# Optimization experiments

Hardware: AMD Instinct MI355X
Metric: run time of the kernel (lower is better)

The kernel has to match this reference:

```python
import jax, jax.numpy as jnp
import numpy as np

E = 100_000      # number of edges
KMAX = 16        # neighbors (quadruplet basis edges) per edge, exact in this setup
E_NB = E * KMAX  # total neighbor entries
D_EDGE, D_SBF, D_QUAD = 128, 32, 32
INV_SQRT_2 = 0.7071067811865475


def setup_inputs() -> dict:
    key = jax.random.key(0)
    ks = jax.random.split(key, 8)
    m_st = jax.random.normal(ks[0], (E, D_EDGE), dtype=jnp.float32)
    sbf = jax.random.normal(ks[1], (E_NB, D_SBF), dtype=jnp.float32)
    # consistent ragged structure: each edge has exactly KMAX neighbor entries
    edge_nb_idx = jnp.repeat(jnp.arange(E, dtype=jnp.int64), KMAX)
    edge_nb_ragged_idx = jnp.tile(jnp.arange(KMAX, dtype=jnp.int64), E)
    idx_swap = jax.random.permutation(ks[2], E).astype(jnp.int64)
    # parameters (Dense layers are bias-free per the module)
    W_down = jax.random.normal(ks[3], (D_EDGE, D_QUAD), dtype=jnp.float32) / np.sqrt(D_EDGE)
    W_bil = jax.random.normal(ks[4], (D_QUAD, D_SBF, D_QUAD), dtype=jnp.float32) / np.sqrt(D_QUAD * D_SBF)
    W_up_st = jax.random.normal(ks[5], (D_QUAD, D_EDGE), dtype=jnp.float32) / np.sqrt(D_QUAD)
    W_up_ts = jax.random.normal(ks[6], (D_QUAD, D_EDGE), dtype=jnp.float32) / np.sqrt(D_QUAD)
    scale_sbf = jnp.ones((1,), dtype=jnp.float32)  # ScaleFactor (fitted scalar, 1.0 at init)
    return {
        "m_st": m_st, "sbf": sbf, "idx_swap": idx_swap,
        "edge_nb_idx": edge_nb_idx, "edge_nb_ragged_idx": edge_nb_ragged_idx,
        "W_down": W_down, "W_bil": W_bil, "W_up_st": W_up_st,
        "W_up_ts": W_up_ts, "scale_sbf": scale_sbf,
    }


def reference(m_st, sbf, idx_swap, edge_nb_idx, edge_nb_ragged_idx,
              W_down, W_bil, W_up_st, W_up_ts, scale_sbf):
    # mlp_down: Dense(no bias) + SiLU  -> (E, Q)
    m = jax.nn.silu(m_st @ W_down)
    # gather edge embeddings to neighbor entries -> (E_NB, Q)
    m_nb = m[edge_nb_idx]
    # EfficientInteractionBilinear: scatter ragged entries into dense
    # (E, Kmax, *) buffers, then bilinear contraction over neighbors.
    m2 = jnp.zeros((E, KMAX, D_QUAD), m.dtype).at[edge_nb_idx, edge_nb_ragged_idx].set(m_nb)
    s2 = jnp.zeros((E, KMAX, D_SBF), sbf.dtype).at[edge_nb_idx, edge_nb_ragged_idx].set(sbf)
    sum_k = jnp.einsum("eks,ekq->esq", s2, m2)           # (E, S, Q)
    x = jnp.einsum("esq,qso->eo", sum_k, W_bil)          # (E, Q)
    # ScaleFactor: multiply by fitted scalar
    x = x * scale_sbf[0]
    # up-projections + SiLU, swap-add, normalize
    x_st = jax.nn.silu(x @ W_up_st)
    x_ts = jax.nn.silu(x @ W_up_ts)[idx_swap]
    return (x_st + x_ts) * INV_SQRT_2
```

## Files before the change

### kernel.cpp

```cpp
#include <hip/hip_runtime.h>
#include <hip/hip_bf16.h>

#define E_EDGES 100000
#define KMAXN   16
#define D_EDGE  128
#define D_SBF   32
#define D_QUAD  32
#define NTILES  6250
#define SP      36

typedef __bf16 bf16x8 __attribute__((ext_vector_type(8)));
typedef float  f32x4  __attribute__((ext_vector_type(4)));

__device__ __forceinline__ float silu_f(float x) {
    return x / (1.0f + __expf(-x));
}

__global__ __launch_bounds__(256) void kprep(
        const float* __restrict__ W_down,
        const float* __restrict__ W_bil,
        __bf16* __restrict__ Wd16,
        __bf16* __restrict__ Wb16)
{
    const int t = blockIdx.x * 256 + threadIdx.x;
    if (t < 4096) {
        const int o   = t & 31;
        const int tmp = t >> 5;
        const int qh  = tmp & 3;
        const int s   = tmp >> 2;
        bf16x8 u;
        #pragma unroll
        for (int ql = 0; ql < 8; ql++)
            u[ql] = (__bf16)W_bil[(qh*8 + ql)*1024 + s*32 + o];
        *(bf16x8*)(Wb16 + (size_t)t * 8) = u;
    } else if (t < 4096 + 512) {
        const int t2   = t - 4096;
        const int n15  = t2 & 15;
        const int quad = (t2 >> 4) & 3;
        const int nt   = (t2 >> 6) & 1;
        const int kk   = t2 >> 7;
        bf16x8 u;
        #pragma unroll
        for (int j = 0; j < 8; j++)
            u[j] = (__bf16)W_down[(kk*32 + quad*8 + j)*32 + nt*16 + n15];
        *(bf16x8*)(Wd16 + (size_t)t2 * 8) = u;
    }
}

__global__ __launch_bounds__(256, 4) void k012_fused(
        const float* __restrict__ sbf,
        const float* __restrict__ m_st,
        const __bf16* __restrict__ Wd16,
        const __bf16* __restrict__ Wb16,
        const float* __restrict__ scale_sbf,
        float* __restrict__ ws_x)
{
    __shared__ __align__(16) float Slds[4][16 * SP];
    __shared__ __align__(16) float Mlds[4][16 * SP];

    const int lane = threadIdx.x & 63;
    const int n15  = lane & 15;
    const int quad = lane >> 4;
    const int wid  = threadIdx.x >> 6;
    const int tile = blockIdx.x * 4 + wid;
    if (tile >= NTILES) return;
    const int eb = tile * 16;
    const int e8 = lane >> 3;
    const int c  = lane & 7;

    float* Sw = Slds[wid];
    float* Mw = Mlds[wid];

    #pragma unroll
    for (int eh = 0; eh < 2; eh++) {
        const float* p = sbf + (size_t)(eb + eh*8 + e8) * (KMAXN * D_SBF) + c * 4;
        float ax = 0.f, ay = 0.f, az = 0.f, aw = 0.f;
        #pragma unroll
        for (int k = 0; k < KMAXN; k++) {
            float4 v = *(const float4*)(p + k * D_SBF);
            ax += v.x; ay += v.y; az += v.z; aw += v.w;
        }
        float4 r = {ax, ay, az, aw};
        *(float4*)(Sw + (eh*8 + e8) * SP + c * 4) = r;
    }

    const bf16x8* Wdq = (const bf16x8*)Wd16;
    const float* arow = m_st + (size_t)(eb + n15) * 128 + quad * 8;
    f32x4 acc0 = {0.f, 0.f, 0.f, 0.f};
    f32x4 acc1 = {0.f, 0.f, 0.f, 0.f};
    #pragma unroll
    for (int kk = 0; kk < 4; kk++) {
        float4 p0 = *(const float4*)(arow + kk*32);
        float4 p1 = *(const float4*)(arow + kk*32 + 4);
        bf16x8 a;
        a[0]=(__bf16)p0.x; a[1]=(__bf16)p0.y; a[2]=(__bf16)p0.z; a[3]=(__bf16)p0.w;
        a[4]=(__bf16)p1.x; a[5]=(__bf16)p1.y; a[6]=(__bf16)p1.z; a[7]=(__bf16)p1.w;
        bf16x8 b0 = Wdq[(kk*2 + 0)*64 + quad*16 + n15];
        bf16x8 b1 = Wdq[(kk*2 + 1)*64 + quad*16 + n15];
        acc0 = __builtin_amdgcn_mfma_f32_16x16x32_bf16(a, b0, acc0, 0, 0, 0);
        acc1 = __builtin_amdgcn_mfma_f32_16x16x32_bf16(a, b1, acc1, 0, 0, 0);
    }
    #pragma unroll
    for (int reg = 0; reg < 4; reg++) {
        Mw[(quad*4 + reg)*SP +      n15] = silu_f(acc0[reg]);
        Mw[(quad*4 + reg)*SP + 16 + n15] = silu_f(acc1[reg]);
    }

    asm volatile("s_waitcnt lgkmcnt(0)" ::: "memory");

    const float* mrow = Mw + n15*SP + quad*8;
    float4 m0 = *(const float4*)mrow;
    float4 m1 = *(const float4*)(mrow + 4);
    float mj[8] = {m0.x, m0.y, m0.z, m0.w, m1.x, m1.y, m1.z, m1.w};
    const float* srow = Sw + n15*SP;
    const bf16x8* Bq = (const bf16x8*)Wb16;

    f32x4 xc0 = {0.f, 0.f, 0.f, 0.f};
    f32x4 xc1 = {0.f, 0.f, 0.f, 0.f};
    #pragma unroll
    for (int kk = 0; kk < 32; kk++) {
        const float sv = srow[kk];
        bf16x8 a;
        #pragma unroll
        for (int j = 0; j < 8; j++) a[j] = (__bf16)(sv * mj[j]);
        bf16x8 b0 = Bq[(kk*4 + quad)*32 +      n15];
        bf16x8 b1 = Bq[(kk*4 + quad)*32 + 16 + n15];
        xc0 = __builtin_amdgcn_mfma_f32_16x16x32_bf16(a, b0, xc0, 0, 0, 0);
        xc1 = __builtin_amdgcn_mfma_f32_16x16x32_bf16(a, b1, xc1, 0, 0, 0);
    }

    const float scale = scale_sbf[0];
    #pragma unroll
    for (int reg = 0; reg < 4; reg++) {
        const int eo = eb + quad*4 + reg;
        ws_x[(size_t)eo*32 +      n15] = xc0[reg] * scale;
        ws_x[(size_t)eo*32 + 16 + n15] = xc1[reg] * scale;
    }
}

__global__ __launch_bounds__(256) void k3_up(
        const float* __restrict__ ws_x,
        const int*   __restrict__ idx_swap,
        const float* __restrict__ W_up_st,
        const float* __restrict__ W_up_ts,
        float* __restrict__ out)
{
    const int lane = threadIdx.x & 63;
    const int n15  = lane & 15;
    const int quad = lane >> 4;
    const int wave = blockIdx.x * 4 + (threadIdx.x >> 6);
    const int nwav = gridDim.x * 4;

    bf16x8 bst[8], bts[8];
    #pragma unroll
    for (int nt = 0; nt < 8; nt++) {
        bf16x8 a, b;
        #pragma unroll
        for (int j = 0; j < 8; j++) {
            a[j] = (__bf16)W_up_st[(quad*8 + j) * 128 + nt*16 + n15];
            b[j] = (__bf16)W_up_ts[(quad*8 + j) * 128 + nt*16 + n15];
        }
        bst[nt] = a; bts[nt] = b;
    }

    const float cinv = 0.70710678118654752440f;

    for (int tile = wave; tile < NTILES; tile += nwav) {
        const int eb = tile * 16;
        const int e  = eb + n15;
        const int esw = idx_swap[e];

        const float* xr = ws_x + (size_t)e   * 32 + quad * 8;
        const float* xs = ws_x + (size_t)esw * 32 + quad * 8;
        float4 r0 = *(const float4*)xr, r1 = *(const float4*)(xr + 4);
        float4 s0 = *(const float4*)xs, s1 = *(const float4*)(xs + 4);

        bf16x8 ast, ats;
        ast[0]=(__bf16)r0.x; ast[1]=(__bf16)r0.y; ast[2]=(__bf16)r0.z; ast[3]=(__bf16)r0.w;
        ast[4]=(__bf16)r1.x; ast[5]=(__bf16)r1.y; ast[6]=(__bf16)r1.z; ast[7]=(__bf16)r1.w;
        ats[0]=(__bf16)s0.x; ats[1]=(__bf16)s0.y; ats[2]=(__bf16)s0.z; ats[3]=(__bf16)s0.w;
        ats[4]=(__bf16)s1.x; ats[5]=(__bf16)s1.y; ats[6]=(__bf16)s1.z; ats[7]=(__bf16)s1.w;

        f32x4 accst[8], accts[8];
        #pragma unroll
        for (int nt = 0; nt < 8; nt++) {
            f32x4 z = {0.f, 0.f, 0.f, 0.f};
            accst[nt] = __builtin_amdgcn_mfma_f32_16x16x32_bf16(ast, bst[nt], z, 0, 0, 0);
            accts[nt] = __builtin_amdgcn_mfma_f32_16x16x32_bf16(ats, bts[nt], z, 0, 0, 0);
        }

        #pragma unroll
        for (int nt = 0; nt < 8; nt++) {
            #pragma unroll
            for (int reg = 0; reg < 4; reg++) {
                const int eo = eb + quad*4 + reg;
                out[(size_t)eo * 128 + nt*16 + n15] =
                    (silu_f(accst[nt][reg]) + silu_f(accts[nt][reg])) * cinv;
            }
        }
    }
}

extern "C" void kernel_launch(void* const* d_in, const int* in_sizes, int n_in,
                              void* d_out, int out_size, void* d_ws, size_t ws_size,
                              hipStream_t stream)
{
    const float* m_st      = (const float*)d_in[0];
    const float* sbf       = (const float*)d_in[1];
    const int*   idx_swap  = (const int*)  d_in[2];
    const float* W_down    = (const float*)d_in[5];
    const float* W_bil     = (const float*)d_in[6];
    const float* W_up_st   = (const float*)d_in[7];
    const float* W_up_ts   = (const float*)d_in[8];
    const float* scale_sbf = (const float*)d_in[9];
    float* out = (float*)d_out;

    const size_t nEQ = (size_t)E_EDGES * D_QUAD;
    float*  ws_x = (float*)d_ws;
    __bf16* Wd16 = (__bf16*)(ws_x + nEQ);
    __bf16* Wb16 = Wd16 + 512 * 8;

    hipLaunchKernelGGL(kprep,      dim3(18),   dim3(256), 0, stream,
                       W_down, W_bil, Wd16, Wb16);
    hipLaunchKernelGGL(k012_fused, dim3(1563), dim3(256), 0, stream,
                       sbf, m_st, Wd16, Wb16, scale_sbf, ws_x);
    hipLaunchKernelGGL(k3_up,      dim3(1024), dim3(256), 0, stream,
                       ws_x, idx_swap, W_up_st, W_up_ts, out);
}
```

Before: 383.5 us.

## Split sbf neighbor-sum into separate streaming kernel before fused bilinear

Moves the reduction of sbf over the 16 neighbors out of the fused MFMA kernel into a standalone, fully parallel kernel that writes per-edge sums to workspace. The fused kernel then loads the 32 summed values per edge straight into registers instead of staging them through LDS. The aim is to let the dominant 205MB sbf stream run at full occupancy, separate from the MFMA kernel's limited occupancy. The cost is an extra launch and an additional round trip of the summed buffer through global memory.

```diff
diff --git a/kernel.cpp b/kernel.cpp
--- a/kernel.cpp
+++ b/kernel.cpp
@@ -14,6 +14,25 @@
 
 __device__ __forceinline__ float silu_f(float x) {
     return x / (1.0f + __expf(-x));
+}
+
+__global__ __launch_bounds__(256) void k0_ssum(
+        const float* __restrict__ sbf,
+        float* __restrict__ ssum)
+{
+    const int tid = blockIdx.x * 256 + threadIdx.x;
+    if (tid >= E_EDGES * 8) return;
+    const int e = tid >> 3;
+    const int c = tid & 7;
+    const float* p = sbf + (size_t)e * (KMAXN * D_SBF) + c * 4;
+    float ax = 0.f, ay = 0.f, az = 0.f, aw = 0.f;
+    #pragma unroll
+    for (int k = 0; k < KMAXN; k++) {
+        float4 v = *(const float4*)(p + k * D_SBF);
+        ax += v.x; ay += v.y; az += v.z; aw += v.w;
+    }
+    float4 r = {ax, ay, az, aw};
+    *(float4*)(ssum + (size_t)e * D_SBF + c * 4) = r;
 }
 
 __global__ __launch_bounds__(256) void kprep(
@@ -47,15 +66,14 @@
     }
 }
 
-__global__ __launch_bounds__(256, 4) void k012_fused(
-        const float* __restrict__ sbf,
+__global__ __launch_bounds__(256, 4) void k12_fused(
+        const float* __restrict__ ssum,
         const float* __restrict__ m_st,
         const __bf16* __restrict__ Wd16,
         const __bf16* __restrict__ Wb16,
         const float* __restrict__ scale_sbf,
         float* __restrict__ ws_x)
 {
-    __shared__ __align__(16) float Slds[4][16 * SP];
     __shared__ __align__(16) float Mlds[4][16 * SP];
 
     const int lane = threadIdx.x & 63;
@@ -65,24 +83,8 @@
     const int tile = blockIdx.x * 4 + wid;
     if (tile >= NTILES) return;
     const int eb = tile * 16;
-    const int e8 = lane >> 3;
-    const int c  = lane & 7;
-
-    float* Sw = Slds[wid];
+
     float* Mw = Mlds[wid];
-
-    #pragma unroll
-    for (int eh = 0; eh < 2; eh++) {
-        const float* p = sbf + (size_t)(eb + eh*8 + e8) * (KMAXN * D_SBF) + c * 4;
-        float ax = 0.f, ay = 0.f, az = 0.f, aw = 0.f;
-        #pragma unroll
-        for (int k = 0; k < KMAXN; k++) {
-            float4 v = *(const float4*)(p + k * D_SBF);
-            ax += v.x; ay += v.y; az += v.z; aw += v.w;
-        }
-        float4 r = {ax, ay, az, aw};
-        *(float4*)(Sw + (eh*8 + e8) * SP + c * 4) = r;
-    }
 
     const bf16x8* Wdq = (const bf16x8*)Wd16;
     const float* arow = m_st + (size_t)(eb + n15) * 128 + quad * 8;
@@ -106,20 +108,27 @@
         Mw[(quad*4 + reg)*SP + 16 + n15] = silu_f(acc1[reg]);
     }
 
+    float ss[32];
+    const float* srow = ssum + (size_t)(eb + n15) * 32;
+    #pragma unroll
+    for (int cc = 0; cc < 8; cc++) {
+        float4 v = *(const float4*)(srow + cc*4);
+        ss[cc*4+0] = v.x; ss[cc*4+1] = v.y; ss[cc*4+2] = v.z; ss[cc*4+3] = v.w;
+    }
+
     asm volatile("s_waitcnt lgkmcnt(0)" ::: "memory");
 
     const float* mrow = Mw + n15*SP + quad*8;
     float4 m0 = *(const float4*)mrow;
     float4 m1 = *(const float4*)(mrow + 4);
     float mj[8] = {m0.x, m0.y, m0.z, m0.w, m1.x, m1.y, m1.z, m1.w};
-    const float* srow = Sw + n15*SP;
     const bf16x8* Bq = (const bf16x8*)Wb16;
 
     f32x4 xc0 = {0.f, 0.f, 0.f, 0.f};
     f32x4 xc1 = {0.f, 0.f, 0.f, 0.f};
     #pragma unroll
     for (int kk = 0; kk < 32; kk++) {
-        const float sv = srow[kk];
+        const float sv = ss[kk];
         bf16x8 a;
         #pragma unroll
         for (int j = 0; j < 8; j++) a[j] = (__bf16)(sv * mj[j]);
@@ -219,11 +228,13 @@
     float*  ws_x = (float*)d_ws;
     __bf16* Wd16 = (__bf16*)(ws_x + nEQ);
     __bf16* Wb16 = Wd16 + 512 * 8;
-
-    hipLaunchKernelGGL(kprep,      dim3(18),   dim3(256), 0, stream,
+    float*  ssum = (float*)(Wb16 + 4096 * 8);
+
+    hipLaunchKernelGGL(k0_ssum,   dim3(3125), dim3(256), 0, stream, sbf, ssum);
+    hipLaunchKernelGGL(kprep,     dim3(18),   dim3(256), 0, stream,
                        W_down, W_bil, Wd16, Wb16);
-    hipLaunchKernelGGL(k012_fused, dim3(1563), dim3(256), 0, stream,
-                       sbf, m_st, Wd16, Wb16, scale_sbf, ws_x);
-    hipLaunchKernelGGL(k3_up,      dim3(1024), dim3(256), 0, stream,
+    hipLaunchKernelGGL(k12_fused, dim3(1563), dim3(256), 0, stream,
+                       ssum, m_st, Wd16, Wb16, scale_sbf, ws_x);
+    hipLaunchKernelGGL(k3_up,     dim3(1024), dim3(256), 0, stream,
                        ws_x, idx_swap, W_up_st, W_up_ts, out);
 }
```

Result: no change. 391.0 us (+2.0%).
